# Optimization experiments

Hardware: AMD Instinct MI355X
Metric: run time of the kernel (lower is better)

Reference implementation:

```python
import jax, jax.numpy as jnp
import numpy as np
import math

EMBED_DIM = 256
NUM_HEADS = 8
FFN_DIM = 1024
EPS = 1e-5


def layer_norm(x, g, b):
    mu = jnp.mean(x, axis=-1, keepdims=True)
    var = jnp.var(x, axis=-1, keepdims=True)
    return (x - mu) / jnp.sqrt(var + EPS) * g + b


def setup_inputs() -> dict:
    key = jax.random.key(0)
    ks = jax.random.split(key, 10)
    B, L, D, F = 4, 2048, EMBED_DIM, FFN_DIM
    x = jax.random.normal(ks[0], (B, L, D), dtype=jnp.float32)
    mask = jnp.ones((B, L), dtype=jnp.int32)
    # FFN params (PyTorch Linear default-ish scale)
    W1 = jax.random.normal(ks[1], (D, F), dtype=jnp.float32) / np.sqrt(D)
    b1 = jnp.zeros((F,), dtype=jnp.float32)
    W2 = jax.random.normal(ks[2], (F, D), dtype=jnp.float32) / np.sqrt(F)
    b2 = jnp.zeros((D,), dtype=jnp.float32)
    g1 = jnp.ones((D,), dtype=jnp.float32)
    be1 = jnp.zeros((D,), dtype=jnp.float32)
    g2 = jnp.ones((D,), dtype=jnp.float32)
    be2 = jnp.zeros((D,), dtype=jnp.float32)
    return {"x": x, "mask": mask, "W1": W1, "b1": b1, "W2": W2, "b2": b2,
            "g1": g1, "be1": be1, "g2": g2, "be2": be2}


def quantum_attention(x, mask):
    B, L, D = x.shape
    H, dk = NUM_HEADS, D // NUM_HEADS
    xh = x.reshape(B, L, H, dk).transpose(0, 2, 1, 3)  # [B,H,L,dk]
    # per-token mean over batch and heads -> [L, dk]
    m = jnp.mean(xh, axis=(0, 1))
    # closed form of the single-qubit RX circuit: P(|1>) = sin^2(angle/2)
    dot = m @ m.T  # [L, L]
    ang = jnp.clip(dot, -math.pi, math.pi)
    scores = jnp.sin(ang * 0.5) ** 2  # [L, L], shared across B and H
    attn = jnp.broadcast_to(scores[None, None], (B, H, L, L))
    attn = jnp.where(mask[:, None, None, :] == 0, -1e9, attn)
    attn = jax.nn.softmax(attn, axis=-1)
    out = jnp.einsum('bhij,bhjd->bhid', attn, xh)  # values are xh itself
    return out.transpose(0, 2, 1, 3).reshape(B, L, D)


def reference(x, mask, W1, b1, W2, b2, g1, be1, g2, be2):
    attn_out = quantum_attention(x, mask)
    h = layer_norm(x + attn_out, g1, be1)
    ffn = jax.nn.relu(h @ W1 + b1) @ W2 + b2
    return layer_norm(h + ffn, g2, be2)
```

## Files before the change

kernel.cpp:

```cpp
#include <hip/hip_runtime.h>
#include <hip/hip_bf16.h>


#define B_ 4
#define L_ 2048
#define D_ 256
#define F_ 1024
#define PI_F 3.14159265358979323846f

typedef __bf16 bf16x8 __attribute__((ext_vector_type(8)));
typedef float floatx4 __attribute__((ext_vector_type(4)));

__device__ __forceinline__ unsigned short f2bf(float f) {
    unsigned int u = __float_as_uint(f);
    u = (u + 0x7FFFu + ((u >> 16) & 1u)) >> 16;
    return (unsigned short)u;
}
__device__ __forceinline__ float bf2f(unsigned short u) {
    union { unsigned int i; float f; } v; v.i = ((unsigned int)u) << 16; return v.f;
}

__device__ __forceinline__ void async_cp16(unsigned short* lds, const unsigned short* g) {
    __builtin_amdgcn_global_load_lds(
        (const __attribute__((address_space(1))) unsigned int*)g,
        (__attribute__((address_space(3))) unsigned int*)lds, 16, 0, 0);
}

__global__ __launch_bounds__(256) void k_prep(const float* __restrict__ x,
                                              const float* __restrict__ W1,
                                              const float* __restrict__ W2,
                                              const int* __restrict__ mask,
                                              unsigned short* __restrict__ mb,
                                              unsigned short* __restrict__ XmT,
                                              unsigned short* __restrict__ W1T,
                                              unsigned short* __restrict__ W2T) {
    int z = blockIdx.z, t = threadIdx.x;
    if (z == 6) {
        if (blockIdx.x >= 4) return;
        int idx = (blockIdx.y * 4 + blockIdx.x) * 256 + t;
        int l = idx >> 5, k = idx & 31;
        float s = 0.f;
#pragma unroll
        for (int b = 0; b < B_; b++) {
            const float* xp = x + ((size_t)(b * L_ + l)) * D_ + k;
#pragma unroll
            for (int h = 0; h < 8; h++) s += xp[h * 32];
        }
        mb[idx] = f2bf(s * (1.f / 32.f));
        return;
    }
    if (z == 7) {
        if (blockIdx.x || blockIdx.y) return;
#pragma unroll
        for (int c = 0; c < 32; c++) {
            int e = c * 256 + t;
            int b = e >> 11, j = e & (L_ - 1);
            XmT[(size_t)(1024 + b) * L_ + j] = mask[b * L_ + j] ? 0x3F80 : 0;
        }
        return;
    }
    const float* in; unsigned short* outp; int R, C; const int* mrow = nullptr; size_t bo = 0;
    if (z < 4) {
        if (blockIdx.x >= 8) return;
        in = x; outp = XmT; R = L_; C = 256; bo = (size_t)z * R * C; mrow = mask + z * L_;
    } else if (z == 4) {
        if (blockIdx.y >= 8) return;
        in = W1; outp = W1T; R = 256; C = 1024;
    } else {
        if (blockIdx.x >= 8 || blockIdx.y >= 32) return;
        in = W2; outp = W2T; R = 1024; C = 256;
    }
    __shared__ float tile[32][33];
    int r0 = blockIdx.y * 32, c0 = blockIdx.x * 32;
    int tx = t & 31, ty = t >> 5;
#pragma unroll
    for (int rr = 0; rr < 4; rr++) {
        int r = ty + rr * 8;
        tile[r][tx] = in[bo + (size_t)(r0 + r) * C + c0 + tx];
    }
    float mfac = 1.f;
    if (mrow) mfac = mrow[r0 + tx] ? 1.f : 0.f;
    __syncthreads();
#pragma unroll
    for (int rr = 0; rr < 4; rr++) {
        int c = ty + rr * 8;
        outp[bo + (size_t)(c0 + c) * R + r0 + tx] = f2bf(tile[tx][c] * mfac);
    }
}

__global__ __launch_bounds__(256) void k_scores_mfma(const unsigned short* __restrict__ mb,
                                                     unsigned short* __restrict__ E) {
    const int t = threadIdx.x, lane = t & 63, wid = t >> 6;
    const int wm = (wid >> 1) * 64, wn = (wid & 1) * 32;
    const int lr = lane & 15, lq = lane >> 4;
    int m0 = blockIdx.y * 128, n0 = blockIdx.x * 64;
    bf16x8 af[4], bfr[2];
#pragma unroll
    for (int i = 0; i < 4; i++)
        af[i] = *(const bf16x8*)(mb + (size_t)(m0 + wm + i * 16 + lr) * 32 + lq * 8);
#pragma unroll
    for (int j = 0; j < 2; j++)
        bfr[j] = *(const bf16x8*)(mb + (size_t)(n0 + wn + j * 16 + lr) * 32 + lq * 8);
    floatx4 acc[4][2];
#pragma unroll
    for (int i = 0; i < 4; i++)
#pragma unroll
        for (int j = 0; j < 2; j++) {
            acc[i][j] = (floatx4){0.f, 0.f, 0.f, 0.f};
            acc[i][j] = __builtin_amdgcn_mfma_f32_16x16x32_bf16(af[i], bfr[j], acc[i][j], 0, 0, 0);
        }
#pragma unroll
    for (int i = 0; i < 4; i++)
#pragma unroll
        for (int j = 0; j < 2; j++)
#pragma unroll
            for (int r = 0; r < 4; r++) {
                int row = m0 + wm + i * 16 + lq * 4 + r;
                int col = n0 + wn + j * 16 + lr;
                float d = fminf(fmaxf(acc[i][j][r], -PI_F), PI_F);
                float sn = __sinf(0.5f * d);
                E[(size_t)row * L_ + col] = f2bf(__expf(sn * sn));
            }
}

__global__ __launch_bounds__(256) void k_av(const unsigned short* __restrict__ E,
                                            const unsigned short* __restrict__ XmT,
                                            float* __restrict__ C) {
    __shared__ __align__(16) unsigned short sA[64 * 64];
    __shared__ __align__(16) unsigned short sB[64 * 64];
    const int t = threadIdx.x, lane = t & 63, wid = t >> 6;
    const int wm = (wid >> 1) * 32, wn = (wid & 1) * 32;
    const int lr = lane & 15, lq = lane >> 4;
    const int lrow8 = lane >> 3, lseg = lane & 7;
    int m0 = blockIdx.y * 64, n0 = blockIdx.x * 64;

    const unsigned short* Ag[2]; unsigned short* sAd[2];
    const unsigned short* Bg[2]; unsigned short* sBd[2];
#pragma unroll
    for (int q = 0; q < 2; q++) {
        int rl = q * 32 + wid * 8 + lrow8;
        int seg = (lseg - rl) & 7;
        Ag[q] = E + (size_t)(m0 + rl) * L_ + seg * 8;
        Bg[q] = XmT + (size_t)(n0 + rl) * L_ + seg * 8;
        sAd[q] = sA + (q * 32 + wid * 8) * 64;
        sBd[q] = sB + (q * 32 + wid * 8) * 64;
    }
    const unsigned short* sAr[2]; int arot[2];
    const unsigned short* sBr[2]; int brot[2];
#pragma unroll
    for (int i = 0; i < 2; i++) { int ar = wm + i * 16 + lr; sAr[i] = sA + ar * 64; arot[i] = lq + ar; }
#pragma unroll
    for (int j = 0; j < 2; j++) { int br = wn + j * 16 + lr; sBr[j] = sB + br * 64; brot[j] = lq + br; }

    floatx4 acc[2][2];
#pragma unroll
    for (int i = 0; i < 2; i++)
#pragma unroll
        for (int j = 0; j < 2; j++) acc[i][j] = (floatx4){0.f, 0.f, 0.f, 0.f};

    for (int k0 = 0; k0 < L_; k0 += 64) {
        __syncthreads();
#pragma unroll
        for (int q = 0; q < 2; q++) { async_cp16(sAd[q], Ag[q] + k0); async_cp16(sBd[q], Bg[q] + k0); }
        __syncthreads();
#pragma unroll
        for (int s = 0; s < 2; s++) {
            bf16x8 af[2], bfr[2];
#pragma unroll
            for (int i = 0; i < 2; i++) af[i] = *(const bf16x8*)(sAr[i] + ((s * 4 + arot[i]) & 7) * 8);
#pragma unroll
            for (int j = 0; j < 2; j++) bfr[j] = *(const bf16x8*)(sBr[j] + ((s * 4 + brot[j]) & 7) * 8);
#pragma unroll
            for (int i = 0; i < 2; i++)
#pragma unroll
                for (int j = 0; j < 2; j++)
                    acc[i][j] = __builtin_amdgcn_mfma_f32_16x16x32_bf16(af[i], bfr[j], acc[i][j], 0, 0, 0);
        }
    }
#pragma unroll
    for (int i = 0; i < 2; i++)
#pragma unroll
        for (int j = 0; j < 2; j++)
#pragma unroll
            for (int r = 0; r < 4; r++) {
                int row = m0 + wm + i * 16 + lq * 4 + r;
                int col = n0 + wn + j * 16 + lr;
                C[(size_t)row * 1088 + col] = acc[i][j][r];
            }
}

__global__ __launch_bounds__(256) void k_ln1(const float* __restrict__ x, const float* __restrict__ C,
                                             const float* __restrict__ g_, const float* __restrict__ be_,
                                             unsigned short* __restrict__ hb) {
    int tok = blockIdx.x, t = threadIdx.x;
    int b = tok >> 11, i = tok & (L_ - 1);
    float rs = C[(size_t)i * 1088 + 1024 + b];
    float v = x[(size_t)tok * D_ + t] + C[(size_t)i * 1088 + b * 256 + t] / rs;
    float s = v, s2 = v * v;
    __shared__ float sm[8];
#pragma unroll
    for (int o = 1; o < 64; o <<= 1) { s += __shfl_xor(s, o); s2 += __shfl_xor(s2, o); }
    if ((t & 63) == 0) { sm[t >> 6] = s; sm[4 + (t >> 6)] = s2; }
    __syncthreads();
    s = sm[0] + sm[1] + sm[2] + sm[3];
    s2 = sm[4] + sm[5] + sm[6] + sm[7];
    float mu = s * (1.f / 256.f);
    float var = s2 * (1.f / 256.f) - mu * mu;
    float r = rsqrtf(var + 1e-5f);
    hb[(size_t)tok * D_ + t] = f2bf((v - mu) * r * g_[t] + be_[t]);
}

__device__ __forceinline__ void mfma_gemm_async(const unsigned short* __restrict__ A,
                                                const unsigned short* __restrict__ Bt,
                                                int K, int m0, int n0,
                                                unsigned short* sA, unsigned short* sB,
                                                floatx4 acc[4][2]) {
    const int t = threadIdx.x;
    const int lane = t & 63, wid = t >> 6;
    const int wm = (wid >> 1) * 64, wn = (wid & 1) * 32;
    const int lr = lane & 15, lq = lane >> 4;
    const int lrow = lane >> 3, lseg = lane & 7;

    const unsigned short* Ag[4]; unsigned short* sAd[4];
#pragma unroll
    for (int q = 0; q < 4; q++) {
        int rl = wid * 32 + q * 8 + lrow;
        int seg = (lseg - rl) & 7;
        Ag[q] = A + (size_t)(m0 + rl) * K + seg * 8;
        sAd[q] = sA + (wid * 32 + q * 8) * 64;
    }
    const unsigned short* Bg[2]; unsigned short* sBd[2];
#pragma unroll
    for (int q = 0; q < 2; q++) {
        int rl = wid * 16 + q * 8 + lrow;
        int seg = (lseg - rl) & 7;
        Bg[q] = Bt + (size_t)(n0 + rl) * K + seg * 8;
        sBd[q] = sB + (wid * 16 + q * 8) * 64;
    }
    int arot[4], brot[2];
    const unsigned short* sAr[4]; const unsigned short* sBr[2];
#pragma unroll
    for (int i = 0; i < 4; i++) { int ar = wm + i * 16 + lr; sAr[i] = sA + ar * 64; arot[i] = lq + ar; }
#pragma unroll
    for (int j = 0; j < 2; j++) { int br = wn + j * 16 + lr; sBr[j] = sB + br * 64; brot[j] = lq + br; }

    for (int k0 = 0; k0 < K; k0 += 64) {
        __syncthreads();
#pragma unroll
        for (int q = 0; q < 4; q++) async_cp16(sAd[q], Ag[q] + k0);
#pragma unroll
        for (int q = 0; q < 2; q++) async_cp16(sBd[q], Bg[q] + k0);
        __syncthreads();
#pragma unroll
        for (int s = 0; s < 2; s++) {
            bf16x8 af[4], bfr[2];
#pragma unroll
            for (int i = 0; i < 4; i++)
                af[i] = *(const bf16x8*)(sAr[i] + ((s * 4 + arot[i]) & 7) * 8);
#pragma unroll
            for (int j = 0; j < 2; j++)
                bfr[j] = *(const bf16x8*)(sBr[j] + ((s * 4 + brot[j]) & 7) * 8);
#pragma unroll
            for (int i = 0; i < 4; i++)
#pragma unroll
                for (int j = 0; j < 2; j++)
                    acc[i][j] = __builtin_amdgcn_mfma_f32_16x16x32_bf16(af[i], bfr[j], acc[i][j], 0, 0, 0);
        }
    }
}

__global__ __launch_bounds__(256) void k_gemm1(const unsigned short* __restrict__ hb,
                                               const unsigned short* __restrict__ W1T,
                                               const float* __restrict__ b1, unsigned short* __restrict__ t1) {
    __shared__ __align__(16) unsigned short sA[128 * 64];
    __shared__ __align__(16) unsigned short sB[64 * 64];
    floatx4 acc[4][2];
#pragma unroll
    for (int i = 0; i < 4; i++)
#pragma unroll
        for (int j = 0; j < 2; j++) acc[i][j] = (floatx4){0.f, 0.f, 0.f, 0.f};
    int m0 = blockIdx.y * 128, n0 = blockIdx.x * 64;
    mfma_gemm_async(hb, W1T, 256, m0, n0, sA, sB, acc);
    const int lane = threadIdx.x & 63, wid = threadIdx.x >> 6;
    const int wm = (wid >> 1) * 64, wn = (wid & 1) * 32;
    const int lr = lane & 15, lq = lane >> 4;
    float bb0 = b1[n0 + wn + lr], bb1 = b1[n0 + wn + 16 + lr];
#pragma unroll
    for (int i = 0; i < 4; i++)
#pragma unroll
        for (int j = 0; j < 2; j++) {
            float bv = j ? bb1 : bb0;
            int col = n0 + wn + j * 16 + lr;
#pragma unroll
            for (int r = 0; r < 4; r++) {
                int row = m0 + wm + i * 16 + lq * 4 + r;
                t1[(size_t)row * 1024 + col] = f2bf(fmaxf(acc[i][j][r] + bv, 0.f));
            }
        }
}

__global__ __launch_bounds__(256) void k_gemm2ln(const unsigned short* __restrict__ t1,
                                                 const unsigned short* __restrict__ W2T,
                                                 const float* __restrict__ b2,
                                                 const unsigned short* __restrict__ hb,
                                                 const float* __restrict__ g_, const float* __restrict__ be_,
                                                 float* __restrict__ out) {
    __shared__ __align__(16) unsigned short sA[32 * 64];
    __shared__ __align__(16) unsigned short sB[256 * 64];
    __shared__ float red[2][32][2];
    const int t = threadIdx.x, lane = t & 63, wid = t >> 6;
    const int wm = (wid >> 1) * 16, wn = (wid & 1) * 128;
    const int lr = lane & 15, lq = lane >> 4;
    const int lrow8 = lane >> 3, lseg = lane & 7;
    int m0 = blockIdx.x * 32;

    int arl = wid * 8 + lrow8;
    const unsigned short* Ag = t1 + (size_t)(m0 + arl) * 1024 + (((lseg - arl) & 7) * 8);
    unsigned short* sAd = sA + (wid * 8) * 64;
    const unsigned short* Bg[8]; unsigned short* sBd[8];
#pragma unroll
    for (int q = 0; q < 8; q++) {
        int rl = q * 32 + wid * 8 + lrow8;
        Bg[q] = W2T + (size_t)rl * 1024 + (((lseg - rl) & 7) * 8);
        sBd[q] = sB + (q * 32 + wid * 8) * 64;
    }
    const unsigned short* sAr = sA + (wm + lr) * 64; int arot = lq + wm + lr;
    const unsigned short* sBr[8]; int brot[8];
#pragma unroll
    for (int j = 0; j < 8; j++) { int br = wn + j * 16 + lr; sBr[j] = sB + br * 64; brot[j] = lq + br; }

    floatx4 acc[8];
#pragma unroll
    for (int j = 0; j < 8; j++) acc[j] = (floatx4){0.f, 0.f, 0.f, 0.f};

    for (int k0 = 0; k0 < 1024; k0 += 64) {
        __syncthreads();
        async_cp16(sAd, Ag + k0);
#pragma unroll
        for (int q = 0; q < 8; q++) async_cp16(sBd[q], Bg[q] + k0);
        __syncthreads();
#pragma unroll
        for (int s = 0; s < 2; s++) {
            bf16x8 af = *(const bf16x8*)(sAr + ((s * 4 + arot) & 7) * 8);
#pragma unroll
            for (int j = 0; j < 8; j++) {
                bf16x8 bfr = *(const bf16x8*)(sBr[j] + ((s * 4 + brot[j]) & 7) * 8);
                acc[j] = __builtin_amdgcn_mfma_f32_16x16x32_bf16(af, bfr, acc[j], 0, 0, 0);
            }
        }
    }
    float psum[4], psq[4];
#pragma unroll
    for (int r = 0; r < 4; r++) { psum[r] = 0.f; psq[r] = 0.f; }
#pragma unroll
    for (int j = 0; j < 8; j++) {
        int col = wn + j * 16 + lr;
        float bv = b2[col];
#pragma unroll
        for (int r = 0; r < 4; r++) {
            int row = m0 + wm + lq * 4 + r;
            float v = acc[j][r] + bv + bf2f(hb[(size_t)row * 256 + col]);
            acc[j][r] = v;
            psum[r] += v; psq[r] += v * v;
        }
    }
#pragma unroll
    for (int o = 1; o < 16; o <<= 1) {
#pragma unroll
        for (int r = 0; r < 4; r++) { psum[r] += __shfl_xor(psum[r], o); psq[r] += __shfl_xor(psq[r], o); }
    }
    if (lr == 0) {
#pragma unroll
        for (int r = 0; r < 4; r++) {
            int lrow = wm + lq * 4 + r;
            red[wid & 1][lrow][0] = psum[r];
            red[wid & 1][lrow][1] = psq[r];
        }
    }
    __syncthreads();
#pragma unroll
    for (int r = 0; r < 4; r++) {
        int lrow = wm + lq * 4 + r;
        float s = red[0][lrow][0] + red[1][lrow][0];
        float s2 = red[0][lrow][1] + red[1][lrow][1];
        float mu = s * (1.f / 256.f);
        float var = s2 * (1.f / 256.f) - mu * mu;
        float rc = rsqrtf(var + 1e-5f);
        int row = m0 + lrow;
#pragma unroll
        for (int j = 0; j < 8; j++) {
            int col = wn + j * 16 + lr;
            out[(size_t)row * 256 + col] = (acc[j][r] - mu) * rc * g_[col] + be_[col];
        }
    }
}

extern "C" void kernel_launch(void* const* d_in, const int* in_sizes, int n_in,
                              void* d_out, int out_size, void* d_ws, size_t ws_size,
                              hipStream_t stream) {
    const float* x   = (const float*)d_in[0];
    const int*  mask = (const int*)d_in[1];
    const float* W1  = (const float*)d_in[2];
    const float* b1  = (const float*)d_in[3];
    const float* W2  = (const float*)d_in[4];
    const float* b2  = (const float*)d_in[5];
    const float* g1  = (const float*)d_in[6];
    const float* be1 = (const float*)d_in[7];
    const float* g2  = (const float*)d_in[8];
    const float* be2 = (const float*)d_in[9];
    float* out = (float*)d_out;

    char* w = (char*)d_ws;
    unsigned short* mb_   = (unsigned short*)w;  w += 65536 * 2;
    unsigned short* E_    = (unsigned short*)w;  w += (size_t)L_ * L_ * 2;
    unsigned short* XmT_  = (unsigned short*)w;  w += (size_t)1088 * L_ * 2;
    unsigned short* W1T_  = (unsigned short*)w;  w += 262144 * 2;
    unsigned short* W2T_  = (unsigned short*)w;  w += 262144 * 2;
    float*          C_    = (float*)w;           w += (size_t)L_ * 1088 * 4;
    unsigned short* hb_   = (unsigned short*)w;  w += (size_t)8192 * 256 * 2;
    unsigned short* t1_   = (unsigned short*)w;  w += (size_t)8192 * 1024 * 2;

    k_prep<<<dim3(32, 64, 8), 256, 0, stream>>>(x, W1, W2, mask, mb_, XmT_, W1T_, W2T_);
    k_scores_mfma<<<dim3(32, 16), 256, 0, stream>>>(mb_, E_);
    k_av<<<dim3(17, 32), 256, 0, stream>>>(E_, XmT_, C_);
    k_ln1<<<B_ * L_, 256, 0, stream>>>(x, C_, g1, be1, hb_);
    k_gemm1<<<dim3(16, 64), 256, 0, stream>>>(hb_, W1T_, b1, t1_);
    k_gemm2ln<<<256, 256, 0, stream>>>(t1_, W2T_, b2, hb_, g2, be2, out);
}
```

Measured before the change: 153.4 us.

## Compact prep grid, bf16 attention output, larger tiles for AV and GEMM1

The prep kernel is relaunched as a flat 1D grid of exactly the blocks it needs, so the old 3D grid's many early-exit blocks are no longer launched. The attention-value GEMM now uses the shared 128x64 async MFMA helper and writes its output in bf16, which halves the intermediate traffic read by the first LayerNorm. GEMM1 moves to 128x128 tiles with a 4x4 accumulator per wave to get more reuse per LDS load. The costs are extra rounding in the attention output and row-sum, higher register pressure, and fewer blocks for GEMM1 and AV.

Result: no change. 150.8 us (-1.7%).

```diff
diff --git a/kernel.cpp b/kernel.cpp
--- a/kernel.cpp
+++ b/kernel.cpp
@@ -34,49 +34,48 @@
                                               unsigned short* __restrict__ XmT,
                                               unsigned short* __restrict__ W1T,
                                               unsigned short* __restrict__ W2T) {
-    int z = blockIdx.z, t = threadIdx.x;
-    if (z == 6) {
-        if (blockIdx.x >= 4) return;
-        int idx = (blockIdx.y * 4 + blockIdx.x) * 256 + t;
-        int l = idx >> 5, k = idx & 31;
-        float s = 0.f;
-#pragma unroll
-        for (int b = 0; b < B_; b++) {
-            const float* xp = x + ((size_t)(b * L_ + l)) * D_ + k;
-#pragma unroll
-            for (int h = 0; h < 8; h++) s += xp[h * 32];
-        }
-        mb[idx] = f2bf(s * (1.f / 32.f));
+    __shared__ float tile[32][33];
+    int r = blockIdx.x, t = threadIdx.x;
+    if (r >= 2560) {
+        if (r < 2816) {
+            int idx = (r - 2560) * 256 + t;
+            int l = idx >> 5, k = idx & 31;
+            float s = 0.f;
+#pragma unroll
+            for (int b = 0; b < B_; b++) {
+                const float* xp = x + ((size_t)(b * L_ + l)) * D_ + k;
+#pragma unroll
+                for (int h = 0; h < 8; h++) s += xp[h * 32];
+            }
+            mb[idx] = f2bf(s * (1.f / 32.f));
+        } else {
+#pragma unroll
+            for (int c = 0; c < 32; c++) {
+                int e = c * 256 + t;
+                int b = e >> 11, j = e & (L_ - 1);
+                XmT[(size_t)(1024 + b) * L_ + j] = mask[b * L_ + j] ? 0x3F80 : 0;
+            }
+        }
         return;
     }
-    if (z == 7) {
-        if (blockIdx.x || blockIdx.y) return;
-#pragma unroll
-        for (int c = 0; c < 32; c++) {
-            int e = c * 256 + t;
-            int b = e >> 11, j = e & (L_ - 1);
-            XmT[(size_t)(1024 + b) * L_ + j] = mask[b * L_ + j] ? 0x3F80 : 0;
-        }
-        return;
-    }
     const float* in; unsigned short* outp; int R, C; const int* mrow = nullptr; size_t bo = 0;
-    if (z < 4) {
-        if (blockIdx.x >= 8) return;
+    int bx, by;
+    if (r < 2048) {
+        int z = r >> 9, rem = r & 511; by = rem >> 3; bx = rem & 7;
         in = x; outp = XmT; R = L_; C = 256; bo = (size_t)z * R * C; mrow = mask + z * L_;
-    } else if (z == 4) {
-        if (blockIdx.y >= 8) return;
+    } else if (r < 2304) {
+        int rem = r - 2048; bx = rem & 31; by = rem >> 5;
         in = W1; outp = W1T; R = 256; C = 1024;
     } else {
-        if (blockIdx.x >= 8 || blockIdx.y >= 32) return;
+        int rem = r - 2304; bx = rem & 7; by = rem >> 3;
         in = W2; outp = W2T; R = 1024; C = 256;
     }
-    __shared__ float tile[32][33];
-    int r0 = blockIdx.y * 32, c0 = blockIdx.x * 32;
+    int r0 = by * 32, c0 = bx * 32;
     int tx = t & 31, ty = t >> 5;
 #pragma unroll
     for (int rr = 0; rr < 4; rr++) {
-        int r = ty + rr * 8;
-        tile[r][tx] = in[bo + (size_t)(r0 + r) * C + c0 + tx];
+        int rw = ty + rr * 8;
+        tile[rw][tx] = in[bo + (size_t)(r0 + rw) * C + c0 + tx];
     }
     float mfac = 1.f;
     if (mrow) mfac = mrow[r0 + tx] ? 1.f : 0.f;
@@ -121,93 +120,6 @@
                 float sn = __sinf(0.5f * d);
                 E[(size_t)row * L_ + col] = f2bf(__expf(sn * sn));
             }
-}
-
-__global__ __launch_bounds__(256) void k_av(const unsigned short* __restrict__ E,
-                                            const unsigned short* __restrict__ XmT,
-                                            float* __restrict__ C) {
-    __shared__ __align__(16) unsigned short sA[64 * 64];
-    __shared__ __align__(16) unsigned short sB[64 * 64];
-    const int t = threadIdx.x, lane = t & 63, wid = t >> 6;
-    const int wm = (wid >> 1) * 32, wn = (wid & 1) * 32;
-    const int lr = lane & 15, lq = lane >> 4;
-    const int lrow8 = lane >> 3, lseg = lane & 7;
-    int m0 = blockIdx.y * 64, n0 = blockIdx.x * 64;
-
-    const unsigned short* Ag[2]; unsigned short* sAd[2];
-    const unsigned short* Bg[2]; unsigned short* sBd[2];
-#pragma unroll
-    for (int q = 0; q < 2; q++) {
-        int rl = q * 32 + wid * 8 + lrow8;
-        int seg = (lseg - rl) & 7;
-        Ag[q] = E + (size_t)(m0 + rl) * L_ + seg * 8;
-        Bg[q] = XmT + (size_t)(n0 + rl) * L_ + seg * 8;
-        sAd[q] = sA + (q * 32 + wid * 8) * 64;
-        sBd[q] = sB + (q * 32 + wid * 8) * 64;
-    }
-    const unsigned short* sAr[2]; int arot[2];
-    const unsigned short* sBr[2]; int brot[2];
-#pragma unroll
-    for (int i = 0; i < 2; i++) { int ar = wm + i * 16 + lr; sAr[i] = sA + ar * 64; arot[i] = lq + ar; }
-#pragma unroll
-    for (int j = 0; j < 2; j++) { int br = wn + j * 16 + lr; sBr[j] = sB + br * 64; brot[j] = lq + br; }
-
-    floatx4 acc[2][2];
-#pragma unroll
-    for (int i = 0; i < 2; i++)
-#pragma unroll
-        for (int j = 0; j < 2; j++) acc[i][j] = (floatx4){0.f, 0.f, 0.f, 0.f};
-
-    for (int k0 = 0; k0 < L_; k0 += 64) {
-        __syncthreads();
-#pragma unroll
-        for (int q = 0; q < 2; q++) { async_cp16(sAd[q], Ag[q] + k0); async_cp16(sBd[q], Bg[q] + k0); }
-        __syncthreads();
-#pragma unroll
-        for (int s = 0; s < 2; s++) {
-            bf16x8 af[2], bfr[2];
-#pragma unroll
-            for (int i = 0; i < 2; i++) af[i] = *(const bf16x8*)(sAr[i] + ((s * 4 + arot[i]) & 7) * 8);
-#pragma unroll
-            for (int j = 0; j < 2; j++) bfr[j] = *(const bf16x8*)(sBr[j] + ((s * 4 + brot[j]) & 7) * 8);
-#pragma unroll
-            for (int i = 0; i < 2; i++)
-#pragma unroll
-                for (int j = 0; j < 2; j++)
-                    acc[i][j] = __builtin_amdgcn_mfma_f32_16x16x32_bf16(af[i], bfr[j], acc[i][j], 0, 0, 0);
-        }
-    }
-#pragma unroll
-    for (int i = 0; i < 2; i++)
-#pragma unroll
-        for (int j = 0; j < 2; j++)
-#pragma unroll
-            for (int r = 0; r < 4; r++) {
-                int row = m0 + wm + i * 16 + lq * 4 + r;
-                int col = n0 + wn + j * 16 + lr;
-                C[(size_t)row * 1088 + col] = acc[i][j][r];
-            }
-}
-
-__global__ __launch_bounds__(256) void k_ln1(const float* __restrict__ x, const float* __restrict__ C,
-                                             const float* __restrict__ g_, const float* __restrict__ be_,
-                                             unsigned short* __restrict__ hb) {
-    int tok = blockIdx.x, t = threadIdx.x;
-    int b = tok >> 11, i = tok & (L_ - 1);
-    float rs = C[(size_t)i * 1088 + 1024 + b];
-    float v = x[(size_t)tok * D_ + t] + C[(size_t)i * 1088 + b * 256 + t] / rs;
-    float s = v, s2 = v * v;
-    __shared__ float sm[8];
-#pragma unroll
-    for (int o = 1; o < 64; o <<= 1) { s += __shfl_xor(s, o); s2 += __shfl_xor(s2, o); }
-    if ((t & 63) == 0) { sm[t >> 6] = s; sm[4 + (t >> 6)] = s2; }
-    __syncthreads();
-    s = sm[0] + sm[1] + sm[2] + sm[3];
-    s2 = sm[4] + sm[5] + sm[6] + sm[7];
-    float mu = s * (1.f / 256.f);
-    float var = s2 * (1.f / 256.f) - mu * mu;
-    float r = rsqrtf(var + 1e-5f);
-    hb[(size_t)tok * D_ + t] = f2bf((v - mu) * r * g_[t] + be_[t]);
 }
 
 __device__ __forceinline__ void mfma_gemm_async(const unsigned short* __restrict__ A,
@@ -269,32 +181,120 @@
     }
 }
 
+__global__ __launch_bounds__(256) void k_av(const unsigned short* __restrict__ E,
+                                            const unsigned short* __restrict__ XmT,
+                                            unsigned short* __restrict__ Cb) {
+    __shared__ __align__(16) unsigned short sA[128 * 64];
+    __shared__ __align__(16) unsigned short sB[64 * 64];
+    floatx4 acc[4][2];
+#pragma unroll
+    for (int i = 0; i < 4; i++)
+#pragma unroll
+        for (int j = 0; j < 2; j++) acc[i][j] = (floatx4){0.f, 0.f, 0.f, 0.f};
+    int m0 = blockIdx.y * 128, n0 = blockIdx.x * 64;
+    mfma_gemm_async(E, XmT, L_, m0, n0, sA, sB, acc);
+    const int lane = threadIdx.x & 63, wid = threadIdx.x >> 6;
+    const int wm = (wid >> 1) * 64, wn = (wid & 1) * 32;
+    const int lr = lane & 15, lq = lane >> 4;
+#pragma unroll
+    for (int i = 0; i < 4; i++)
+#pragma unroll
+        for (int j = 0; j < 2; j++)
+#pragma unroll
+            for (int r = 0; r < 4; r++) {
+                int row = m0 + wm + i * 16 + lq * 4 + r;
+                int col = n0 + wn + j * 16 + lr;
+                Cb[(size_t)row * 1088 + col] = f2bf(acc[i][j][r]);
+            }
+}
+
+__global__ __launch_bounds__(256) void k_ln1(const float* __restrict__ x, const unsigned short* __restrict__ Cb,
+                                             const float* __restrict__ g_, const float* __restrict__ be_,
+                                             unsigned short* __restrict__ hb) {
+    int tok = blockIdx.x, t = threadIdx.x;
+    int b = tok >> 11, i = tok & (L_ - 1);
+    float rs = bf2f(Cb[(size_t)i * 1088 + 1024 + b]);
+    float v = x[(size_t)tok * D_ + t] + bf2f(Cb[(size_t)i * 1088 + b * 256 + t]) / rs;
+    float s = v, s2 = v * v;
+    __shared__ float sm[8];
+#pragma unroll
+    for (int o = 1; o < 64; o <<= 1) { s += __shfl_xor(s, o); s2 += __shfl_xor(s2, o); }
+    if ((t & 63) == 0) { sm[t >> 6] = s; sm[4 + (t >> 6)] = s2; }
+    __syncthreads();
+    s = sm[0] + sm[1] + sm[2] + sm[3];
+    s2 = sm[4] + sm[5] + sm[6] + sm[7];
+    float mu = s * (1.f / 256.f);
+    float var = s2 * (1.f / 256.f) - mu * mu;
+    float r = rsqrtf(var + 1e-5f);
+    hb[(size_t)tok * D_ + t] = f2bf((v - mu) * r * g_[t] + be_[t]);
+}
+
 __global__ __launch_bounds__(256) void k_gemm1(const unsigned short* __restrict__ hb,
                                                const unsigned short* __restrict__ W1T,
                                                const float* __restrict__ b1, unsigned short* __restrict__ t1) {
     __shared__ __align__(16) unsigned short sA[128 * 64];
-    __shared__ __align__(16) unsigned short sB[64 * 64];
-    floatx4 acc[4][2];
-#pragma unroll
-    for (int i = 0; i < 4; i++)
-#pragma unroll
-        for (int j = 0; j < 2; j++) acc[i][j] = (floatx4){0.f, 0.f, 0.f, 0.f};
-    int m0 = blockIdx.y * 128, n0 = blockIdx.x * 64;
-    mfma_gemm_async(hb, W1T, 256, m0, n0, sA, sB, acc);
-    const int lane = threadIdx.x & 63, wid = threadIdx.x >> 6;
-    const int wm = (wid >> 1) * 64, wn = (wid & 1) * 32;
+    __shared__ __align__(16) unsigned short sB[128 * 64];
+    const int t = threadIdx.x, lane = t & 63, wid = t >> 6;
+    const int wm = (wid >> 1) * 64, wn = (wid & 1) * 64;
     const int lr = lane & 15, lq = lane >> 4;
-    float bb0 = b1[n0 + wn + lr], bb1 = b1[n0 + wn + 16 + lr];
-#pragma unroll
-    for (int i = 0; i < 4; i++)
-#pragma unroll
-        for (int j = 0; j < 2; j++) {
-            float bv = j ? bb1 : bb0;
+    const int lrow8 = lane >> 3, lseg = lane & 7;
+    int m0 = blockIdx.y * 128, n0 = blockIdx.x * 128;
+
+    const unsigned short* Ag[4]; unsigned short* sAd[4];
+    const unsigned short* Bg[4]; unsigned short* sBd[4];
+#pragma unroll
+    for (int q = 0; q < 4; q++) {
+        int rl = q * 32 + wid * 8 + lrow8;
+        int seg = (lseg - rl) & 7;
+        Ag[q] = hb + (size_t)(m0 + rl) * 256 + seg * 8;
+        Bg[q] = W1T + (size_t)(n0 + rl) * 256 + seg * 8;
+        sAd[q] = sA + (q * 32 + wid * 8) * 64;
+        sBd[q] = sB + (q * 32 + wid * 8) * 64;
+    }
+    const unsigned short* sAr[4]; int arot[4];
+    const unsigned short* sBr[4]; int brot[4];
+#pragma unroll
+    for (int i = 0; i < 4; i++) { int ar = wm + i * 16 + lr; sAr[i] = sA + ar * 64; arot[i] = lq + ar; }
+#pragma unroll
+    for (int j = 0; j < 4; j++) { int br = wn + j * 16 + lr; sBr[j] = sB + br * 64; brot[j] = lq + br; }
+
+    floatx4 acc[4][4];
+#pragma unroll
+    for (int i = 0; i < 4; i++)
+#pragma unroll
+        for (int j = 0; j < 4; j++) acc[i][j] = (floatx4){0.f, 0.f, 0.f, 0.f};
+
+    for (int k0 = 0; k0 < 256; k0 += 64) {
+        __syncthreads();
+#pragma unroll
+        for (int q = 0; q < 4; q++) { async_cp16(sAd[q], Ag[q] + k0); async_cp16(sBd[q], Bg[q] + k0); }
+        __syncthreads();
+#pragma unroll
+        for (int s = 0; s < 2; s++) {
+            bf16x8 af[4], bfr[4];
+#pragma unroll
+            for (int i = 0; i < 4; i++) af[i] = *(const bf16x8*)(sAr[i] + ((s * 4 + arot[i]) & 7) * 8);
+#pragma unroll
+            for (int j = 0; j < 4; j++) bfr[j] = *(const bf16x8*)(sBr[j] + ((s * 4 + brot[j]) & 7) * 8);
+#pragma unroll
+            for (int i = 0; i < 4; i++)
+#pragma unroll
+                for (int j = 0; j < 4; j++)
+                    acc[i][j] = __builtin_amdgcn_mfma_f32_16x16x32_bf16(af[i], bfr[j], acc[i][j], 0, 0, 0);
+        }
+    }
+    float bb[4];
+#pragma unroll
+    for (int j = 0; j < 4; j++) bb[j] = b1[n0 + wn + j * 16 + lr];
+#pragma unroll
+    for (int i = 0; i < 4; i++)
+#pragma unroll
+        for (int j = 0; j < 4; j++) {
             int col = n0 + wn + j * 16 + lr;
 #pragma unroll
             for (int r = 0; r < 4; r++) {
                 int row = m0 + wm + i * 16 + lq * 4 + r;
-                t1[(size_t)row * 1024 + col] = f2bf(fmaxf(acc[i][j][r] + bv, 0.f));
+                t1[(size_t)row * 1024 + col] = f2bf(fmaxf(acc[i][j][r] + bb[j], 0.f));
             }
         }
 }
@@ -416,14 +416,14 @@
     unsigned short* XmT_  = (unsigned short*)w;  w += (size_t)1088 * L_ * 2;
     unsigned short* W1T_  = (unsigned short*)w;  w += 262144 * 2;
     unsigned short* W2T_  = (unsigned short*)w;  w += 262144 * 2;
-    float*          C_    = (float*)w;           w += (size_t)L_ * 1088 * 4;
+    unsigned short* Cb_   = (unsigned short*)w;  w += (size_t)L_ * 1088 * 2;
     unsigned short* hb_   = (unsigned short*)w;  w += (size_t)8192 * 256 * 2;
     unsigned short* t1_   = (unsigned short*)w;  w += (size_t)8192 * 1024 * 2;
 
-    k_prep<<<dim3(32, 64, 8), 256, 0, stream>>>(x, W1, W2, mask, mb_, XmT_, W1T_, W2T_);
+    k_prep<<<2817, 256, 0, stream>>>(x, W1, W2, mask, mb_, XmT_, W1T_, W2T_);
     k_scores_mfma<<<dim3(32, 16), 256, 0, stream>>>(mb_, E_);
-    k_av<<<dim3(17, 32), 256, 0, stream>>>(E_, XmT_, C_);
-    k_ln1<<<B_ * L_, 256, 0, stream>>>(x, C_, g1, be1, hb_);
-    k_gemm1<<<dim3(16, 64), 256, 0, stream>>>(hb_, W1T_, b1, t1_);
+    k_av<<<dim3(17, 16), 256, 0, stream>>>(E_, XmT_, Cb_);
+    k_ln1<<<B_ * L_, 256, 0, stream>>>(x, Cb_, g1, be1, hb_);
+    k_gemm1<<<dim3(8, 64), 256, 0, stream>>>(hb_, W1T_, b1, t1_);
     k_gemm2ln<<<256, 256, 0, stream>>>(t1_, W2T_, b2, hb_, g2, be2, out);
 }
```
